# Kernel tuning notes

Measured on AMD Instinct MI355X. Metric: run time of the kernel, lower is better.

Reference implementation:

```python
import jax, jax.numpy as jnp
import numpy as np

B, L, D_MODEL, D_INNER, D_CONV = 4, 4096, 1024, 2048, 4


def setup_inputs() -> dict:
    key = jax.random.key(0)
    ks = jax.random.split(key, 9)
    r = lambda k, shape, s: jax.random.normal(k, shape, dtype=jnp.float32) * s
    return {
        "x": r(ks[0], (B, L, D_MODEL), 1.0),
        "Wi": r(ks[1], (2 * D_INNER, D_MODEL), 0.02),        # in_proj (no bias)
        "Wconv": r(ks[2], (D_INNER, 1, D_CONV), 0.2),        # depthwise conv1d weight
        "bconv": r(ks[3], (D_INNER,), 0.02),                 # conv1d bias
        "Wdt": r(ks[4], (D_INNER, D_INNER), 0.01),           # dt_proj weight
        "bdt": jnp.full((D_INNER,), -3.0, jnp.float32),     # dt_proj bias -> small dt
        "WB": r(ks[5], (D_INNER, D_INNER), 0.02),            # B_proj
        "WC": r(ks[6], (D_INNER, D_INNER), 0.02),            # C_proj
        "Wo": r(ks[7], (D_MODEL, D_INNER), 0.02),            # out_proj
        "A_log": jnp.log(jnp.full((D_INNER,), 0.1, jnp.float32)),
    }


def reference(x, Wi, Wconv, bconv, Wdt, bdt, WB, WC, Wo, A_log):
    L_ = x.shape[1]
    d_conv = Wconv.shape[-1]
    d_inner = Wconv.shape[0]

    # in_proj and gate split
    xz = jnp.einsum('bld,ed->ble', x, Wi)          # [B, L, 2*d_inner]
    x1, z = jnp.split(xz, 2, axis=-1)

    # depthwise causal conv1d (padding=d_conv-1 then truncate == left-pad only)
    xc = jax.lax.conv_general_dilated(
        jnp.transpose(x1, (0, 2, 1)), Wconv,
        window_strides=(1,), padding=[(d_conv - 1, 0)],
        dimension_numbers=('NCH', 'OIH', 'NCH'),
        feature_group_count=d_inner) + bconv[None, :, None]
    xc = jnp.transpose(jax.nn.silu(xc), (0, 2, 1))  # [B, L, d_inner]

    dt = jax.nn.softplus(jnp.einsum('ble,fe->blf', xc, Wdt) + bdt)
    B_t = jax.nn.sigmoid(jnp.einsum('ble,fe->blf', xc, WB))
    C_t = jnp.tanh(jnp.einsum('ble,fe->blf', xc, WC))
    u_t = xc * B_t

    A = -jnp.exp(A_log)                              # [d_inner], negative
    log_alpha = jnp.clip(A[None, None, :] * dt, -10.0, -0.0001)
    S = jnp.cumsum(log_alpha, axis=1)                # [B, L, d_inner]

    u_prev = jnp.concatenate([jnp.zeros_like(u_t[:, :1]), u_t[:, :-1]], axis=1)
    beta = dt * 0.5 * (u_prev + u_t)                 # trapezoid input term

    # stabilized log-cumsum-exp style parallel scan
    m = jnp.max(-S, axis=1, keepdims=True)
    h = jnp.exp(S + m) * jnp.cumsum(beta * jnp.exp(-S - m), axis=1)

    y = h * C_t * jax.nn.silu(z)
    return jnp.einsum('blf,df->bld', y, Wo)
```

## Files before the change

### kernel.cpp

```cpp
#include <hip/hip_runtime.h>
#include <cstdint>

typedef unsigned short u16;
typedef unsigned int u32;
typedef __bf16 bf16x8 __attribute__((ext_vector_type(8)));
typedef float f32x4 __attribute__((ext_vector_type(4)));
typedef unsigned short u16x8 __attribute__((ext_vector_type(8)));

#define BM 128
#define BN 128
#define BK 32
#define PL (BM * BK)
#define CL 32
#define NC 128
#define VCH 8
#define DI 2048
#define DM 1024
#define LSEQ 4096

__device__ __forceinline__ float bf2f(u16 u) {
    union { uint32_t i; float f; } v; v.i = ((uint32_t)u) << 16; return v.f;
}
__device__ __forceinline__ u16 f2bf(float f) {
    union { float f; uint32_t i; } v; v.f = f;
    uint32_t r = v.i + 0x7fffu + ((v.i >> 16) & 1u);
    return (u16)(r >> 16);
}

__device__ __forceinline__ void gl_lds16(const u16* g, u16* l) {
    __builtin_amdgcn_global_load_lds(
        (const __attribute__((address_space(1))) u32*)g,
        (__attribute__((address_space(3))) u32*)l, 16, 0, 0);
}

__global__ __launch_bounds__(256)
void cast_f2b(const float* __restrict__ src, u16* __restrict__ dst, long n)
{
    long i = ((long)blockIdx.x * 256 + threadIdx.x) * 8;
    if (i >= n) return;
    float4 v0 = *(const float4*)(src + i);
    float4 v1 = *(const float4*)(src + i + 4);
    u16x8 o;
    o[0] = f2bf(v0.x); o[1] = f2bf(v0.y); o[2] = f2bf(v0.z); o[3] = f2bf(v0.w);
    o[4] = f2bf(v1.x); o[5] = f2bf(v1.y); o[6] = f2bf(v1.z); o[7] = f2bf(v1.w);
    *(u16x8*)(dst + i) = o;
}

__global__ __launch_bounds__(256)
void cast_weights(const float* __restrict__ Wi, const float* __restrict__ Wdt,
                  const float* __restrict__ WB, const float* __restrict__ WC,
                  const float* __restrict__ Wo,
                  u16* __restrict__ Wi_b, u16* __restrict__ Wcat_b,
                  u16* __restrict__ Wo_b)
{
    const long nWi = (long)2 * DI * DM;
    const long nWp = (long)DI * DI;
    long i = ((long)blockIdx.x * 256 + threadIdx.x) * 8;
    const float* src; u16* dst; long off;
    if (i < nWi)                  { src = Wi;  dst = Wi_b;            off = i; }
    else if (i < nWi + nWp)       { src = Wdt; dst = Wcat_b;          off = i - nWi; }
    else if (i < nWi + 2 * nWp)   { src = WB;  dst = Wcat_b + nWp;    off = i - nWi - nWp; }
    else if (i < nWi + 3 * nWp)   { src = WC;  dst = Wcat_b + 2*nWp;  off = i - nWi - 2*nWp; }
    else                          { src = Wo;  dst = Wo_b;            off = i - nWi - 3*nWp; }
    float4 v0 = *(const float4*)(src + off);
    float4 v1 = *(const float4*)(src + off + 4);
    u16x8 o;
    o[0] = f2bf(v0.x); o[1] = f2bf(v0.y); o[2] = f2bf(v0.z); o[3] = f2bf(v0.w);
    o[4] = f2bf(v1.x); o[5] = f2bf(v1.y); o[6] = f2bf(v1.z); o[7] = f2bf(v1.w);
    *(u16x8*)(dst + off) = o;
}

template<int EPI>
__device__ __forceinline__ void gemm_body(
             const u16* __restrict__ A, const u16* __restrict__ W, int K,
             const float* __restrict__ auxf, const u16* __restrict__ auxb,
             u16* __restrict__ ob0, u16* __restrict__ ob1,
             u16* __restrict__ ob2, float* __restrict__ outf)
{
    __shared__ __align__(16) u16 As[2 * BM * BK];
    __shared__ __align__(16) u16 Bs[2 * BN * BK];

    const int t    = threadIdx.x;
    const int lane = t & 63;
    const int w    = t >> 6;
    const int quad = lane >> 4;
    const int l16  = lane & 15;
    const int wm   = w >> 1, wn = w & 1;
    const long m0  = (long)blockIdx.y * BM;
    const long n0  = (long)blockIdx.x * BN;

    const int rr = lane >> 2;
    const int cg = ((lane & 3) - ((lane >> 3) & 3)) & 3;

    const u16* gA0 = A + (size_t)(m0 + (2 * w)     * 16 + rr) * K + cg * 8;
    const u16* gA1 = A + (size_t)(m0 + (2 * w + 1) * 16 + rr) * K + cg * 8;
    const u16* gB0 = W + (size_t)(n0 + (2 * w)     * 16 + rr) * K + cg * 8;
    const u16* gB1 = W + (size_t)(n0 + (2 * w + 1) * 16 + rr) * K + cg * 8;

    u16* lA0 = As + (2 * w)     * 512;
    u16* lA1 = As + (2 * w + 1) * 512;
    u16* lB0 = Bs + (2 * w)     * 512;
    u16* lB1 = Bs + (2 * w + 1) * 512;

    const int slotr = (quad + (l16 >> 1)) & 3;
    const u16* rdA = As + (wm * 64 + l16) * 32 + slotr * 8;
    const u16* rdB = Bs + (wn * 64 + l16) * 32 + slotr * 8;

    f32x4 acc[4][4];
#pragma unroll
    for (int i = 0; i < 4; ++i)
#pragma unroll
        for (int j = 0; j < 4; ++j)
            acc[i][j] = (f32x4){0.f, 0.f, 0.f, 0.f};

    for (int k0 = 0; k0 < K; k0 += 2 * BK) {
        __syncthreads();
        gl_lds16(gA0 + k0, lA0);
        gl_lds16(gA1 + k0, lA1);
        gl_lds16(gA0 + k0 + BK, lA0 + PL);
        gl_lds16(gA1 + k0 + BK, lA1 + PL);
        gl_lds16(gB0 + k0, lB0);
        gl_lds16(gB1 + k0, lB1);
        gl_lds16(gB0 + k0 + BK, lB0 + PL);
        gl_lds16(gB1 + k0 + BK, lB1 + PL);
        __syncthreads();

#pragma unroll
        for (int kk = 0; kk < 2; ++kk) {
            const u16* pA = rdA + kk * PL;
            const u16* pB = rdB + kk * PL;
            bf16x8 af[4], bfr[4];
#pragma unroll
            for (int fi = 0; fi < 4; ++fi)
                af[fi] = *(const bf16x8*)(pA + fi * 512);
#pragma unroll
            for (int fj = 0; fj < 4; ++fj)
                bfr[fj] = *(const bf16x8*)(pB + fj * 512);
#pragma unroll
            for (int i = 0; i < 4; ++i)
#pragma unroll
                for (int j = 0; j < 4; ++j)
                    acc[i][j] = __builtin_amdgcn_mfma_f32_16x16x32_bf16(af[i], bfr[j], acc[i][j], 0, 0, 0);
        }
    }

#pragma unroll
    for (int i = 0; i < 4; ++i) {
#pragma unroll
        for (int j = 0; j < 4; ++j) {
            const long nc = n0 + wn * 64 + j * 16 + l16;
#pragma unroll
            for (int rg = 0; rg < 4; ++rg) {
                const long mr = m0 + wm * 64 + i * 16 + quad * 4 + rg;
                float v = acc[i][j][rg];
                if (EPI == 0) {
                    if (nc < DI) ob0[mr * DI + nc] = f2bf(v);
                    else         ob1[mr * DI + (nc - DI)] = f2bf(v);
                } else if (EPI == 1) {
                    const int  g   = (int)(nc >> 11);
                    const long col = nc & (DI - 1);
                    if (g == 0) {
                        v += auxf[col];
                        float sp = (v > 20.f) ? v : log1pf(expf(v));
                        ob0[mr * DI + col] = f2bf(sp);
                    } else if (g == 1) {
                        float bt  = 1.f / (1.f + expf(-v));
                        float xcv = bf2f(auxb[mr * DI + col]);
                        ob1[mr * DI + col] = f2bf(xcv * bt);
                    } else {
                        ob2[mr * DI + col] = f2bf(tanhf(v));
                    }
                } else {
                    outf[mr * DM + nc] = v;
                }
            }
        }
    }
}

__global__ __launch_bounds__(256, 4)
void gemm_in(const u16* __restrict__ A, const u16* __restrict__ W, int K,
             u16* __restrict__ ob0, u16* __restrict__ ob1)
{
    gemm_body<0>(A, W, K, nullptr, nullptr, ob0, ob1, nullptr, nullptr);
}
__global__ __launch_bounds__(256, 4)
void gemm_dbc(const u16* __restrict__ A, const u16* __restrict__ W, int K,
              const float* __restrict__ auxf, const u16* __restrict__ auxb,
              u16* __restrict__ ob0, u16* __restrict__ ob1, u16* __restrict__ ob2)
{
    gemm_body<1>(A, W, K, auxf, auxb, ob0, ob1, ob2, nullptr);
}
__global__ __launch_bounds__(256, 4)
void gemm_out(const u16* __restrict__ A, const u16* __restrict__ W, int K,
              float* __restrict__ outf)
{
    gemm_body<2>(A, W, K, nullptr, nullptr, nullptr, nullptr, nullptr, outf);
}

__global__ __launch_bounds__(256)
void conv_silu(const u16* __restrict__ x1, const float* __restrict__ Wc,
               const float* __restrict__ bc, u16* __restrict__ xc)
{
    const long bl = blockIdx.x;
    const int  l  = (int)(bl & (LSEQ - 1));
    const int  d0 = threadIdx.x * VCH;
    const size_t base = (size_t)bl * DI + d0;

    float acc[VCH];
    {
        float4 b0 = *(const float4*)(bc + d0);
        float4 b1 = *(const float4*)(bc + d0 + 4);
        acc[0] = b0.x; acc[1] = b0.y; acc[2] = b0.z; acc[3] = b0.w;
        acc[4] = b1.x; acc[5] = b1.y; acc[6] = b1.z; acc[7] = b1.w;
    }
    float wv[VCH][4];
#pragma unroll
    for (int v = 0; v < VCH; ++v) {
        float4 t = *(const float4*)(Wc + (size_t)(d0 + v) * 4);
        wv[v][0] = t.x; wv[v][1] = t.y; wv[v][2] = t.z; wv[v][3] = t.w;
    }

#pragma unroll
    for (int tp = 0; tp < 4; ++tp) {
        const int ls = l - 3 + tp;
        if (ls >= 0) {
            u16x8 vx = *(const u16x8*)(x1 + base + (long)(tp - 3) * DI);
#pragma unroll
            for (int v = 0; v < VCH; ++v)
                acc[v] += bf2f(vx[v]) * wv[v][tp];
        }
    }
    u16x8 o;
#pragma unroll
    for (int v = 0; v < VCH; ++v) {
        float s = acc[v] / (1.f + expf(-acc[v]));
        o[v] = f2bf(s);
    }
    *(u16x8*)(xc + base) = o;
}

__global__ __launch_bounds__(256)
void scan_a(const u16* __restrict__ dt, const u16* __restrict__ u,
            const float* __restrict__ A_log,
            float* __restrict__ sumlog, float* __restrict__ hend, int nbD)
{
    const int d0 = threadIdx.x * VCH;
    const int b  = blockIdx.y;
    const int c  = blockIdx.z;
    float Ad[VCH];
    {
        float4 a0 = *(const float4*)(A_log + d0);
        float4 a1 = *(const float4*)(A_log + d0 + 4);
        Ad[0] = -expf(a0.x); Ad[1] = -expf(a0.y); Ad[2] = -expf(a0.z); Ad[3] = -expf(a0.w);
        Ad[4] = -expf(a1.x); Ad[5] = -expf(a1.y); Ad[6] = -expf(a1.z); Ad[7] = -expf(a1.w);
    }
    size_t base = ((size_t)b * LSEQ + (size_t)c * CL) * DI + d0;

    float pu[VCH], sl[VCH], h[VCH];
    if (c == 0) {
#pragma unroll
        for (int v = 0; v < VCH; ++v) pu[v] = 0.f;
    } else {
        u16x8 vp = *(const u16x8*)(u + base - DI);
#pragma unroll
        for (int v = 0; v < VCH; ++v) pu[v] = bf2f(vp[v]);
    }
#pragma unroll
    for (int v = 0; v < VCH; ++v) { sl[v] = 0.f; h[v] = 0.f; }

    u16x8 vdt = *(const u16x8*)(dt + base);
    u16x8 vu  = *(const u16x8*)(u  + base);
    for (int s = 0; s < CL; ++s) {
        u16x8 ndt = *(const u16x8*)(dt + base + DI);
        u16x8 nu  = *(const u16x8*)(u  + base + DI);
#pragma unroll
        for (int v = 0; v < VCH; ++v) {
            float dtv = bf2f(vdt[v]);
            float uv  = bf2f(vu[v]);
            float la  = fminf(fmaxf(Ad[v] * dtv, -10.f), -1e-4f);
            sl[v] += la;
            h[v] = expf(la) * h[v] + dtv * 0.5f * (pu[v] + uv);
            pu[v] = uv;
        }
        vdt = ndt; vu = nu;
        base += DI;
    }
    const size_t chn = (size_t)c * nbD + b * DI + d0;
    *(float4*)(sumlog + chn)     = (float4){sl[0], sl[1], sl[2], sl[3]};
    *(float4*)(sumlog + chn + 4) = (float4){sl[4], sl[5], sl[6], sl[7]};
    *(float4*)(hend   + chn)     = (float4){h[0], h[1], h[2], h[3]};
    *(float4*)(hend   + chn + 4) = (float4){h[4], h[5], h[6], h[7]};
}

__global__ __launch_bounds__(256)
void scan_b(const float* __restrict__ sumlog, const float* __restrict__ hend,
            float* __restrict__ hin, int nbD)
{
    const int chn = blockIdx.x * 256 + threadIdx.x;
    float carry = 0.f;
#pragma unroll 4
    for (int c = 0; c < NC; ++c) {
        hin[(size_t)c * nbD + chn] = carry;
        carry = expf(sumlog[(size_t)c * nbD + chn]) * carry + hend[(size_t)c * nbD + chn];
    }
}

__global__ __launch_bounds__(256)
void scan_c(const u16* __restrict__ dt, const u16* __restrict__ u,
            const float* __restrict__ A_log, const float* __restrict__ hin,
            const u16* __restrict__ Ct, const u16* __restrict__ z,
            u16* __restrict__ y, int nbD)
{
    const int d0 = threadIdx.x * VCH;
    const int b  = blockIdx.y;
    const int c  = blockIdx.z;
    float Ad[VCH];
    {
        float4 a0 = *(const float4*)(A_log + d0);
        float4 a1 = *(const float4*)(A_log + d0 + 4);
        Ad[0] = -expf(a0.x); Ad[1] = -expf(a0.y); Ad[2] = -expf(a0.z); Ad[3] = -expf(a0.w);
        Ad[4] = -expf(a1.x); Ad[5] = -expf(a1.y); Ad[6] = -expf(a1.z); Ad[7] = -expf(a1.w);
    }
    size_t base = ((size_t)b * LSEQ + (size_t)c * CL) * DI + d0;
    const size_t chn = (size_t)c * nbD + b * DI + d0;

    float h[VCH], pu[VCH];
    {
        float4 h0 = *(const float4*)(hin + chn);
        float4 h1 = *(const float4*)(hin + chn + 4);
        h[0] = h0.x; h[1] = h0.y; h[2] = h0.z; h[3] = h0.w;
        h[4] = h1.x; h[5] = h1.y; h[6] = h1.z; h[7] = h1.w;
    }
    if (c == 0) {
#pragma unroll
        for (int v = 0; v < VCH; ++v) pu[v] = 0.f;
    } else {
        u16x8 vp = *(const u16x8*)(u + base - DI);
#pragma unroll
        for (int v = 0; v < VCH; ++v) pu[v] = bf2f(vp[v]);
    }

    u16x8 vdt = *(const u16x8*)(dt + base);
    u16x8 vu  = *(const u16x8*)(u  + base);
    u16x8 vct = *(const u16x8*)(Ct + base);
    u16x8 vz  = *(const u16x8*)(z  + base);
    for (int s = 0; s < CL; ++s) {
        u16x8 ndt = *(const u16x8*)(dt + base + DI);
        u16x8 nu  = *(const u16x8*)(u  + base + DI);
        u16x8 nct = *(const u16x8*)(Ct + base + DI);
        u16x8 nz  = *(const u16x8*)(z  + base + DI);
        u16x8 o;
#pragma unroll
        for (int v = 0; v < VCH; ++v) {
            float dtv = bf2f(vdt[v]);
            float uv  = bf2f(vu[v]);
            float la  = fminf(fmaxf(Ad[v] * dtv, -10.f), -1e-4f);
            h[v] = expf(la) * h[v] + dtv * 0.5f * (pu[v] + uv);
            pu[v] = uv;
            float ct = bf2f(vct[v]);
            float zv = bf2f(vz[v]);
            float sz = zv / (1.f + expf(-zv));
            o[v] = f2bf(h[v] * ct * sz);
        }
        *(u16x8*)(y + base) = o;
        vdt = ndt; vu = nu; vct = nct; vz = nz;
        base += DI;
    }
}

struct WeightsB {
    const u16 *Wi, *Wcat, *Wo;
};
struct SmallF {
    const float *Wconv, *bconv, *bdt, *A_log;
};

static void run_pipeline(int nb, const float* x, float* out, char* ws,
                         const WeightsB& wb, const SmallF& sf, hipStream_t stream)
{
    const int Mrows = nb * LSEQ;
    const size_t nE = (size_t)Mrows * DI;
    const size_t nX = (size_t)Mrows * DM;
    const int nbD = nb * DI;

    char* p = ws;
    u16* b0 = (u16*)p; p += nE * 2;
    u16* b1 = (u16*)p; p += nE * 2;
    u16* b2 = (u16*)p; p += nE * 2;
    u16* b3 = (u16*)p; p += nE * 2;
    u16* b4 = (u16*)p; p += nE * 2;

    u16* xb = b2;
    u16* x1 = b0; u16* z = b1; u16* xc = b2;
    u16* dt = b0; u16* u  = b3; u16* Ct = b4; u16* y = b4;

    float* sumlog = (float*)b2;
    float* hend   = sumlog + (size_t)nbD * NC;
    float* hin    = hend   + (size_t)nbD * NC;

    dim3 blk(256);

    cast_f2b<<<dim3((unsigned)(nX / 2048)), blk, 0, stream>>>(x, xb, (long)nX);

    gemm_in<<<dim3(2 * DI / BN, Mrows / BM), blk, 0, stream>>>(
        xb, wb.Wi, DM, x1, z);

    conv_silu<<<dim3((unsigned)Mrows), blk, 0, stream>>>(x1, sf.Wconv, sf.bconv, xc);

    gemm_dbc<<<dim3(3 * DI / BN, Mrows / BM), blk, 0, stream>>>(
        xc, wb.Wcat, DI, sf.bdt, xc, dt, u, Ct);

    scan_a<<<dim3(1, nb, NC), blk, 0, stream>>>(dt, u, sf.A_log, sumlog, hend, nbD);
    scan_b<<<dim3(nbD / 256), blk, 0, stream>>>(sumlog, hend, hin, nbD);
    scan_c<<<dim3(1, nb, NC), blk, 0, stream>>>(dt, u, sf.A_log, hin, Ct, z, y, nbD);

    gemm_out<<<dim3(DM / BN, Mrows / BM), blk, 0, stream>>>(
        y, wb.Wo, DI, out);
}

extern "C" void kernel_launch(void* const* d_in, const int* in_sizes, int n_in,
                              void* d_out, int out_size, void* d_ws, size_t ws_size,
                              hipStream_t stream)
{
    const float* x     = (const float*)d_in[0];
    const float* Wi    = (const float*)d_in[1];
    const float* Wconv = (const float*)d_in[2];
    const float* bconv = (const float*)d_in[3];
    const float* Wdt   = (const float*)d_in[4];
    const float* bdt   = (const float*)d_in[5];
    const float* WB    = (const float*)d_in[6];
    const float* WC    = (const float*)d_in[7];
    const float* Wo    = (const float*)d_in[8];
    const float* A_log = (const float*)d_in[9];

    const size_t nWi = (size_t)2 * DI * DM;
    const size_t nWp = (size_t)DI * DI;
    const size_t nWo = (size_t)DM * DI;

    const size_t wbytes = (nWi + 3 * nWp + nWo) * 2;
    char* q = (char*)d_ws + ws_size - wbytes;
    u16* Wi_b   = (u16*)q; q += nWi * 2;
    u16* Wcat_b = (u16*)q; q += 3 * nWp * 2;
    u16* Wo_b   = (u16*)q; q += nWo * 2;

    dim3 blk(256);
    {
        const long nW = (long)(nWi + 3 * nWp + nWo);
        cast_weights<<<dim3((unsigned)(nW / 2048)), blk, 0, stream>>>(
            Wi, Wdt, WB, WC, Wo, Wi_b, Wcat_b, Wo_b);
    }

    WeightsB wb{Wi_b, Wcat_b, Wo_b};
    SmallF   sf{Wconv, bconv, bdt, A_log};

    auto need = [&](int nb) -> size_t {
        size_t nE = (size_t)nb * LSEQ * DI;
        return 5 * nE * 2;
    };

    if (ws_size >= need(4) + wbytes) {
        run_pipeline(4, x, (float*)d_out, (char*)d_ws, wb, sf, stream);
    } else if (ws_size >= need(2) + wbytes) {
        for (int b = 0; b < 4; b += 2)
            run_pipeline(2, x + (size_t)b * LSEQ * DM,
                         (float*)d_out + (size_t)b * LSEQ * DM,
                         (char*)d_ws, wb, sf, stream);
    } else {
        for (int b = 0; b < 4; ++b)
            run_pipeline(1, x + (size_t)b * LSEQ * DM,
                         (float*)d_out + (size_t)b * LSEQ * DM,
                         (char*)d_ws, wb, sf, stream);
    }
}
```

Baseline: 1.271 ms.

## Increase scan parallelism with smaller chunks and narrower per-thread vectors

```diff
diff --git a/kernel.cpp b/kernel.cpp
--- a/kernel.cpp
+++ b/kernel.cpp
@@ -6,14 +6,14 @@
 typedef __bf16 bf16x8 __attribute__((ext_vector_type(8)));
 typedef float f32x4 __attribute__((ext_vector_type(4)));
 typedef unsigned short u16x8 __attribute__((ext_vector_type(8)));
+typedef unsigned short u16x4 __attribute__((ext_vector_type(4)));
 
 #define BM 128
 #define BN 128
 #define BK 32
 #define PL (BM * BK)
-#define CL 32
-#define NC 128
-#define VCH 8
+#define CL 16
+#define NC 256
 #define DI 2048
 #define DM 1024
 #define LSEQ 4096
@@ -204,19 +204,19 @@
 {
     const long bl = blockIdx.x;
     const int  l  = (int)(bl & (LSEQ - 1));
-    const int  d0 = threadIdx.x * VCH;
+    const int  d0 = threadIdx.x * 8;
     const size_t base = (size_t)bl * DI + d0;
 
-    float acc[VCH];
+    float acc[8];
     {
         float4 b0 = *(const float4*)(bc + d0);
         float4 b1 = *(const float4*)(bc + d0 + 4);
         acc[0] = b0.x; acc[1] = b0.y; acc[2] = b0.z; acc[3] = b0.w;
         acc[4] = b1.x; acc[5] = b1.y; acc[6] = b1.z; acc[7] = b1.w;
     }
-    float wv[VCH][4];
-#pragma unroll
-    for (int v = 0; v < VCH; ++v) {
+    float wv[8][4];
+#pragma unroll
+    for (int v = 0; v < 8; ++v) {
         float4 t = *(const float4*)(Wc + (size_t)(d0 + v) * 4);
         wv[v][0] = t.x; wv[v][1] = t.y; wv[v][2] = t.z; wv[v][3] = t.w;
     }
@@ -227,13 +227,13 @@
         if (ls >= 0) {
             u16x8 vx = *(const u16x8*)(x1 + base + (long)(tp - 3) * DI);
 #pragma unroll
-            for (int v = 0; v < VCH; ++v)
+            for (int v = 0; v < 8; ++v)
                 acc[v] += bf2f(vx[v]) * wv[v][tp];
         }
     }
     u16x8 o;
 #pragma unroll
-    for (int v = 0; v < VCH; ++v) {
+    for (int v = 0; v < 8; ++v) {
         float s = acc[v] / (1.f + expf(-acc[v]));
         o[v] = f2bf(s);
     }
@@ -245,64 +245,73 @@
             const float* __restrict__ A_log,
             float* __restrict__ sumlog, float* __restrict__ hend, int nbD)
 {
-    const int d0 = threadIdx.x * VCH;
+    const int d0 = (blockIdx.x * 256 + threadIdx.x) * 4;
     const int b  = blockIdx.y;
     const int c  = blockIdx.z;
-    float Ad[VCH];
+    float Ad[4];
     {
-        float4 a0 = *(const float4*)(A_log + d0);
-        float4 a1 = *(const float4*)(A_log + d0 + 4);
-        Ad[0] = -expf(a0.x); Ad[1] = -expf(a0.y); Ad[2] = -expf(a0.z); Ad[3] = -expf(a0.w);
-        Ad[4] = -expf(a1.x); Ad[5] = -expf(a1.y); Ad[6] = -expf(a1.z); Ad[7] = -expf(a1.w);
+        float4 a = *(const float4*)(A_log + d0);
+        Ad[0] = -expf(a.x); Ad[1] = -expf(a.y); Ad[2] = -expf(a.z); Ad[3] = -expf(a.w);
     }
     size_t base = ((size_t)b * LSEQ + (size_t)c * CL) * DI + d0;
 
-    float pu[VCH], sl[VCH], h[VCH];
+    float pu[4], sl[4], h[4];
     if (c == 0) {
 #pragma unroll
-        for (int v = 0; v < VCH; ++v) pu[v] = 0.f;
+        for (int v = 0; v < 4; ++v) pu[v] = 0.f;
     } else {
-        u16x8 vp = *(const u16x8*)(u + base - DI);
-#pragma unroll
-        for (int v = 0; v < VCH; ++v) pu[v] = bf2f(vp[v]);
-    }
-#pragma unroll
-    for (int v = 0; v < VCH; ++v) { sl[v] = 0.f; h[v] = 0.f; }
-
-    u16x8 vdt = *(const u16x8*)(dt + base);
-    u16x8 vu  = *(const u16x8*)(u  + base);
+        u16x4 vp = *(const u16x4*)(u + base - DI);
+#pragma unroll
+        for (int v = 0; v < 4; ++v) pu[v] = bf2f(vp[v]);
+    }
+#pragma unroll
+    for (int v = 0; v < 4; ++v) { sl[v] = 0.f; h[v] = 0.f; }
+
+    u16x4 d_0 = *(const u16x4*)(dt + base);
+    u16x4 u_0 = *(const u16x4*)(u  + base);
+    u16x4 d_1 = *(const u16x4*)(dt + base + DI);
+    u16x4 u_1 = *(const u16x4*)(u  + base + DI);
     for (int s = 0; s < CL; ++s) {
-        u16x8 ndt = *(const u16x8*)(dt + base + DI);
-        u16x8 nu  = *(const u16x8*)(u  + base + DI);
-#pragma unroll
-        for (int v = 0; v < VCH; ++v) {
-            float dtv = bf2f(vdt[v]);
-            float uv  = bf2f(vu[v]);
+        u16x4 d_2 = *(const u16x4*)(dt + base + 2 * DI);
+        u16x4 u_2 = *(const u16x4*)(u  + base + 2 * DI);
+#pragma unroll
+        for (int v = 0; v < 4; ++v) {
+            float dtv = bf2f(d_0[v]);
+            float uv  = bf2f(u_0[v]);
             float la  = fminf(fmaxf(Ad[v] * dtv, -10.f), -1e-4f);
             sl[v] += la;
             h[v] = expf(la) * h[v] + dtv * 0.5f * (pu[v] + uv);
             pu[v] = uv;
         }
-        vdt = ndt; vu = nu;
+        d_0 = d_1; u_0 = u_1; d_1 = d_2; u_1 = u_2;
         base += DI;
     }
     const size_t chn = (size_t)c * nbD + b * DI + d0;
-    *(float4*)(sumlog + chn)     = (float4){sl[0], sl[1], sl[2], sl[3]};
-    *(float4*)(sumlog + chn + 4) = (float4){sl[4], sl[5], sl[6], sl[7]};
-    *(float4*)(hend   + chn)     = (float4){h[0], h[1], h[2], h[3]};
-    *(float4*)(hend   + chn + 4) = (float4){h[4], h[5], h[6], h[7]};
-}
-
-__global__ __launch_bounds__(256)
+    *(float4*)(sumlog + chn) = (float4){sl[0], sl[1], sl[2], sl[3]};
+    *(float4*)(hend   + chn) = (float4){h[0], h[1], h[2], h[3]};
+}
+
+__global__ __launch_bounds__(128)
 void scan_b(const float* __restrict__ sumlog, const float* __restrict__ hend,
             float* __restrict__ hin, int nbD)
 {
-    const int chn = blockIdx.x * 256 + threadIdx.x;
+    const int chn = blockIdx.x * 128 + threadIdx.x;
     float carry = 0.f;
-#pragma unroll 4
-    for (int c = 0; c < NC; ++c) {
-        hin[(size_t)c * nbD + chn] = carry;
-        carry = expf(sumlog[(size_t)c * nbD + chn]) * carry + hend[(size_t)c * nbD + chn];
+    for (int c0 = 0; c0 < NC; c0 += 8) {
+        float sl[8], he[8];
+#pragma unroll
+        for (int k = 0; k < 8; ++k) {
+            sl[k] = sumlog[(size_t)(c0 + k) * nbD + chn];
+            he[k] = hend  [(size_t)(c0 + k) * nbD + chn];
+        }
+        float e[8];
+#pragma unroll
+        for (int k = 0; k < 8; ++k) e[k] = expf(sl[k]);
+#pragma unroll
+        for (int k = 0; k < 8; ++k) {
+            hin[(size_t)(c0 + k) * nbD + chn] = carry;
+            carry = e[k] * carry + he[k];
+        }
     }
 }
 
@@ -312,59 +321,60 @@
             const u16* __restrict__ Ct, const u16* __restrict__ z,
             u16* __restrict__ y, int nbD)
 {
-    const int d0 = threadIdx.x * VCH;
+    const int d0 = (blockIdx.x * 256 + threadIdx.x) * 4;
     const int b  = blockIdx.y;
     const int c  = blockIdx.z;
-    float Ad[VCH];
+    float Ad[4];
     {
-        float4 a0 = *(const float4*)(A_log + d0);
-        float4 a1 = *(const float4*)(A_log + d0 + 4);
-        Ad[0] = -expf(a0.x); Ad[1] = -expf(a0.y); Ad[2] = -expf(a0.z); Ad[3] = -expf(a0.w);
-        Ad[4] = -expf(a1.x); Ad[5] = -expf(a1.y); Ad[6] = -expf(a1.z); Ad[7] = -expf(a1.w);
+        float4 a = *(const float4*)(A_log + d0);
+        Ad[0] = -expf(a.x); Ad[1] = -expf(a.y); Ad[2] = -expf(a.z); Ad[3] = -expf(a.w);
     }
     size_t base = ((size_t)b * LSEQ + (size_t)c * CL) * DI + d0;
     const size_t chn = (size_t)c * nbD + b * DI + d0;
 
-    float h[VCH], pu[VCH];
+    float h[4], pu[4];
     {
-        float4 h0 = *(const float4*)(hin + chn);
-        float4 h1 = *(const float4*)(hin + chn + 4);
-        h[0] = h0.x; h[1] = h0.y; h[2] = h0.z; h[3] = h0.w;
-        h[4] = h1.x; h[5] = h1.y; h[6] = h1.z; h[7] = h1.w;
+        float4 h4 = *(const float4*)(hin + chn);
+        h[0] = h4.x; h[1] = h4.y; h[2] = h4.z; h[3] = h4.w;
     }
     if (c == 0) {
 #pragma unroll
-        for (int v = 0; v < VCH; ++v) pu[v] = 0.f;
+        for (int v = 0; v < 4; ++v) pu[v] = 0.f;
     } else {
-        u16x8 vp = *(const u16x8*)(u + base - DI);
-#pragma unroll
-        for (int v = 0; v < VCH; ++v) pu[v] = bf2f(vp[v]);
-    }
-
-    u16x8 vdt = *(const u16x8*)(dt + base);
-    u16x8 vu  = *(const u16x8*)(u  + base);
-    u16x8 vct = *(const u16x8*)(Ct + base);
-    u16x8 vz  = *(const u16x8*)(z  + base);
+        u16x4 vp = *(const u16x4*)(u + base - DI);
+#pragma unroll
+        for (int v = 0; v < 4; ++v) pu[v] = bf2f(vp[v]);
+    }
+
+    u16x4 d_0 = *(const u16x4*)(dt + base);
+    u16x4 u_0 = *(const u16x4*)(u  + base);
+    u16x4 c_0 = *(const u16x4*)(Ct + base);
+    u16x4 z_0 = *(const u16x4*)(z  + base);
+    u16x4 d_1 = *(const u16x4*)(dt + base + DI);
+    u16x4 u_1 = *(const u16x4*)(u  + base + DI);
+    u16x4 c_1 = *(const u16x4*)(Ct + base + DI);
+    u16x4 z_1 = *(const u16x4*)(z  + base + DI);
     for (int s = 0; s < CL; ++s) {
-        u16x8 ndt = *(const u16x8*)(dt + base + DI);
-        u16x8 nu  = *(const u16x8*)(u  + base + DI);
-        u16x8 nct = *(const u16x8*)(Ct + base + DI);
-        u16x8 nz  = *(const u16x8*)(z  + base + DI);
-        u16x8 o;
-#pragma unroll
-        for (int v = 0; v < VCH; ++v) {
-            float dtv = bf2f(vdt[v]);
-            float uv  = bf2f(vu[v]);
+        u16x4 d_2 = *(const u16x4*)(dt + base + 2 * DI);
+        u16x4 u_2 = *(const u16x4*)(u  + base + 2 * DI);
+        u16x4 c_2 = *(const u16x4*)(Ct + base + 2 * DI);
+        u16x4 z_2 = *(const u16x4*)(z  + base + 2 * DI);
+        u16x4 o;
+#pragma unroll
+        for (int v = 0; v < 4; ++v) {
+            float dtv = bf2f(d_0[v]);
+            float uv  = bf2f(u_0[v]);
             float la  = fminf(fmaxf(Ad[v] * dtv, -10.f), -1e-4f);
             h[v] = expf(la) * h[v] + dtv * 0.5f * (pu[v] + uv);
             pu[v] = uv;
-            float ct = bf2f(vct[v]);
-            float zv = bf2f(vz[v]);
+            float ct = bf2f(c_0[v]);
+            float zv = bf2f(z_0[v]);
             float sz = zv / (1.f + expf(-zv));
             o[v] = f2bf(h[v] * ct * sz);
         }
-        *(u16x8*)(y + base) = o;
-        vdt = ndt; vu = nu; vct = nct; vz = nz;
+        *(u16x4*)(y + base) = o;
+        d_0 = d_1; u_0 = u_1; c_0 = c_1; z_0 = z_1;
+        d_1 = d_2; u_1 = u_2; c_1 = c_2; z_1 = z_2;
         base += DI;
     }
 }
@@ -411,9 +421,9 @@
     gemm_dbc<<<dim3(3 * DI / BN, Mrows / BM), blk, 0, stream>>>(
         xc, wb.Wcat, DI, sf.bdt, xc, dt, u, Ct);
 
-    scan_a<<<dim3(1, nb, NC), blk, 0, stream>>>(dt, u, sf.A_log, sumlog, hend, nbD);
-    scan_b<<<dim3(nbD / 256), blk, 0, stream>>>(sumlog, hend, hin, nbD);
-    scan_c<<<dim3(1, nb, NC), blk, 0, stream>>>(dt, u, sf.A_log, hin, Ct, z, y, nbD);
+    scan_a<<<dim3(2, nb, NC), blk, 0, stream>>>(dt, u, sf.A_log, sumlog, hend, nbD);
+    scan_b<<<dim3(nbD / 128), dim3(128), 0, stream>>>(sumlog, hend, hin, nbD);
+    scan_c<<<dim3(2, nb, NC), blk, 0, stream>>>(dt, u, sf.A_log, hin, Ct, z, y, nbD);
 
     gemm_out<<<dim3(DM / BN, Mrows / BM), blk, 0, stream>>>(
         y, wb.Wo, DI, out);
```

After: 1.284 ms. Within noise of the previous version (+1.0%).
